# Kernel optimization log

Hardware: AMD Instinct MI355X
Metric: run time of the kernel (lower is better)

## Reference

```python
import jax, jax.numpy as jnp
import numpy as np

GROUPS = 32
EPS = 1e-5
N_HEADS = 4


def group_norm(x, w, b):
    # x: [B, C, T]; GroupNorm over (C/G, T) within each of G groups
    B, C, T = x.shape
    xg = x.reshape(B, GROUPS, (C // GROUPS) * T)
    mean = xg.mean(axis=-1, keepdims=True)
    var = xg.var(axis=-1, keepdims=True)
    xn = ((xg - mean) * jax.lax.rsqrt(var + EPS)).reshape(B, C, T)
    return xn * w[None, :, None] + b[None, :, None]


def setup_inputs() -> dict:
    key = jax.random.key(0)
    ks = jax.random.split(key, 5)
    B, C, H, W = 2, 256, 64, 64
    x = jax.random.normal(ks[0], (B, C, H, W), dtype=jnp.float32)
    norm_w = jnp.ones((C,), dtype=jnp.float32)
    norm_b = jnp.zeros((C,), dtype=jnp.float32)
    qkv_w = jax.random.normal(ks[1], (3 * C, C), dtype=jnp.float32) * (C ** -0.5)
    qkv_b = jax.random.normal(ks[2], (3 * C,), dtype=jnp.float32) * 0.02
    proj_w = jax.random.normal(ks[3], (C, C), dtype=jnp.float32) * (C ** -0.5)
    proj_b = jax.random.normal(ks[4], (C,), dtype=jnp.float32) * 0.02
    return {"x": x, "norm_w": norm_w, "norm_b": norm_b,
            "qkv_w": qkv_w, "qkv_b": qkv_b,
            "proj_w": proj_w, "proj_b": proj_b}


def reference(x, norm_w, norm_b, qkv_w, qkv_b, proj_w, proj_b):
    B, C, Hs, Ws = x.shape
    T = Hs * Ws
    xf = x.reshape(B, C, T)
    xn = group_norm(xf, norm_w, norm_b)
    # 1x1 conv1d == channel matmul: [3C,C] x [B,C,T] -> [B,3C,T]
    qkv = jnp.einsum('oc,bct->bot', qkv_w, xn) + qkv_b[None, :, None]
    ch = C // N_HEADS
    # legacy order: [B, H*3*ch, T] -> [B*H, 3*ch, T] -> split
    qkv_h = qkv.reshape(B * N_HEADS, 3 * ch, T)
    q, k, v = qkv_h[:, :ch], qkv_h[:, ch:2 * ch], qkv_h[:, 2 * ch:]
    scale = ch ** -0.25
    # full [B*H, T, T] score matrix, softmax in fp32 (faithful to source)
    weight = jnp.einsum('bct,bcs->bts', q * scale, k * scale)
    weight = jax.nn.softmax(weight.astype(jnp.float32), axis=-1).astype(qkv.dtype)
    a = jnp.einsum('bts,bcs->bct', weight, v).reshape(B, C, T)
    h = jnp.einsum('oc,bct->bot', proj_w, a) + proj_b[None, :, None]
    return (xf + h).reshape(B, C, Hs, Ws)
```

## Files before the change

kernel.cpp:

```cpp
#include <hip/hip_runtime.h>
#include <hip/hip_bf16.h>

#define B_    2
#define C_    256
#define T_    4096
#define GRP   32
#define CPG   8
#define NH    4
#define CH    64
#define K3C   768
#define SPLIT 4
#define GSL   8
#define NSTAT (B_ * GRP * GSL)
#define NCVT  128
#define LOG2E 1.4426950408889634f

typedef __attribute__((ext_vector_type(8))) short bf16x8;
typedef __attribute__((ext_vector_type(4))) float f32x4;

#if __has_builtin(__builtin_amdgcn_exp2f)
#define EXP2(x) __builtin_amdgcn_exp2f(x)
#else
#define EXP2(x) exp2f(x)
#endif

__device__ __forceinline__ unsigned pk2(float a, float b) {
    __hip_bfloat162 h = __float22bfloat162_rn(make_float2(a, b));
    union { __hip_bfloat162 h2; unsigned u; } cv; cv.h2 = h;
    return cv.u;
}
__device__ __forceinline__ float bf2f(unsigned short u) {
    return __uint_as_float((unsigned)u << 16);
}

__global__ __launch_bounds__(256) void pre_kernel(
    const float* __restrict__ x, float* __restrict__ stat,
    const float* __restrict__ qw, const float* __restrict__ pw,
    unsigned short* __restrict__ qwb, unsigned short* __restrict__ pwb) {
    int bid = blockIdx.x;
    int tid = threadIdx.x;
    if (bid < NSTAT) {
        int bg = bid >> 3, sl = bid & 7;
        const int SLN = CPG * T_ / GSL;
        const float* xp = x + (size_t)bg * CPG * T_ + (size_t)sl * SLN;
        float s = 0.f, s2 = 0.f;
        for (int i = tid * 4; i < SLN; i += 1024) {
            float4 v = *(const float4*)&xp[i];
            s  += (v.x + v.y) + (v.z + v.w);
            s2 += (v.x * v.x + v.y * v.y) + (v.z * v.z + v.w * v.w);
        }
        for (int off = 32; off > 0; off >>= 1) {
            s  += __shfl_down(s,  off);
            s2 += __shfl_down(s2, off);
        }
        __shared__ float rs[4], rs2[4];
        int wid = tid >> 6;
        if ((tid & 63) == 0) { rs[wid] = s; rs2[wid] = s2; }
        __syncthreads();
        if (tid == 0) {
            stat[bid * 2]     = (rs[0] + rs[1]) + (rs[2] + rs[3]);
            stat[bid * 2 + 1] = (rs2[0] + rs2[1]) + (rs2[2] + rs2[3]);
        }
    } else {
        int i = (bid - NSTAT) * 256 + tid;
        const int n1 = K3C * C_ / 8;
        const float* src; unsigned short* dst;
        if (i < n1) { src = qw + 8 * i; dst = qwb + 8 * i; }
        else { int j = i - n1; src = pw + 8 * j; dst = pwb + 8 * j; }
        float4 a = *(const float4*)src;
        float4 b = *(const float4*)(src + 4);
        uint4 u;
        u.x = pk2(a.x, a.y); u.y = pk2(a.z, a.w);
        u.z = pk2(b.x, b.y); u.w = pk2(b.z, b.w);
        *(uint4*)dst = u;
    }
}

__global__ __launch_bounds__(256) void gn_apply_kernel(
    const float* __restrict__ x, const float* __restrict__ stat,
    const float* __restrict__ w, const float* __restrict__ b,
    unsigned short* __restrict__ xnT) {
    int bg = blockIdx.x, sl = blockIdx.y;
    int batch = bg / GRP, g = bg % GRP;
    const float* xp = x + (size_t)bg * CPG * T_;
    int tid = threadIdx.x;

    float s = 0.f, s2 = 0.f;
#pragma unroll
    for (int i = 0; i < GSL; ++i) {
        s  += stat[(bg * GSL + i) * 2];
        s2 += stat[(bg * GSL + i) * 2 + 1];
    }
    float inv_n = 1.f / (float)(CPG * T_);
    float mean = s * inv_n;
    float var  = s2 * inv_n - mean * mean;
    float inv  = rsqrtf(var + 1e-5f);

    float wv[8], bv[8];
#pragma unroll
    for (int j = 0; j < 8; j++) {
        float ww = w[g * CPG + j] * inv;
        wv[j] = ww;
        bv[j] = b[g * CPG + j] - mean * ww;
    }
    unsigned short* op = xnT + (size_t)batch * T_ * C_ + g * CPG;
    int t0 = sl * (T_ / GSL);
#pragma unroll
    for (int rep = 0; rep < 2; ++rep) {
        int t = t0 + rep * 256 + tid;
        float v[8];
#pragma unroll
        for (int j = 0; j < 8; j++) v[j] = xp[(size_t)j * T_ + t] * wv[j] + bv[j];
        uint4 u;
        u.x = pk2(v[0], v[1]); u.y = pk2(v[2], v[3]);
        u.z = pk2(v[4], v[5]); u.w = pk2(v[6], v[7]);
        *(uint4*)&op[(size_t)t * C_] = u;
    }
}

__global__ __launch_bounds__(256) void qkv_gemm_kernel(
    const unsigned short* __restrict__ Wb, const float* __restrict__ bias,
    const unsigned short* __restrict__ Xt, unsigned short* __restrict__ q_t,
    unsigned short* __restrict__ k_t, unsigned short* __restrict__ v_d) {
    int tb = blockIdx.x * 128;
    int by = blockIdx.y;
    int bz = blockIdx.z;
    int ob = by * 64;
    int tid = threadIdx.x;
    int l = tid & 15, oct = (tid >> 4) & 3, w = tid >> 6;

    __shared__ __align__(16) unsigned short SH[64 * 264];

#pragma unroll
    for (int j = 0; j < 8; ++j) {
        int idx = tid + 256 * j;
        int row = idx >> 5, ch = idx & 31;
        *(uint4*)&SH[row * 264 + ch * 8] =
            *(const uint4*)&Wb[(size_t)(ob + row) * C_ + ch * 8];
    }
    __syncthreads();

    const unsigned short* Xb = Xt + (size_t)bz * T_ * C_;

    f32x4 acc[4][2];
#pragma unroll
    for (int mf = 0; mf < 4; ++mf)
#pragma unroll
        for (int nf = 0; nf < 2; ++nf) acc[mf][nf] = (f32x4){0.f, 0.f, 0.f, 0.f};

#pragma unroll
    for (int kk = 0; kk < 8; ++kk) {
        int c0 = 32 * kk + 8 * oct;
        bf16x8 bfr[2];
#pragma unroll
        for (int nf = 0; nf < 2; ++nf)
            bfr[nf] = *(const bf16x8*)&Xb[(size_t)(tb + 32 * w + 16 * nf + l) * C_ + c0];
#pragma unroll
        for (int mf = 0; mf < 4; ++mf) {
            bf16x8 af = *(const bf16x8*)&SH[(16 * mf + l) * 264 + c0];
#pragma unroll
            for (int nf = 0; nf < 2; ++nf)
                acc[mf][nf] = __builtin_amdgcn_mfma_f32_16x16x32_bf16(af, bfr[nf], acc[mf][nf], 0, 0, 0);
        }
    }

    int head = by / 3, sec = by - 3 * head;
    int bh = bz * NH + head;

    if (sec < 2) {
        float scale = (sec == 0) ? 0.125f * LOG2E : 1.f;
        unsigned short* dst = ((sec == 0) ? q_t : k_t) + (size_t)bh * T_ * CH;
#pragma unroll
        for (int mf = 0; mf < 4; ++mf) {
            float bvs[4];
#pragma unroll
            for (int r = 0; r < 4; ++r) bvs[r] = bias[ob + 16 * mf + 4 * oct + r];
#pragma unroll
            for (int nf = 0; nf < 2; ++nf) {
                int t = tb + 32 * w + 16 * nf + l;
                float v0 = (acc[mf][nf][0] + bvs[0]) * scale;
                float v1 = (acc[mf][nf][1] + bvs[1]) * scale;
                float v2 = (acc[mf][nf][2] + bvs[2]) * scale;
                float v3 = (acc[mf][nf][3] + bvs[3]) * scale;
                uint2 u; u.x = pk2(v0, v1); u.y = pk2(v2, v3);
                *(uint2*)&dst[(size_t)t * CH + 16 * mf + 4 * oct] = u;
            }
        }
    } else {
        __syncthreads();
#pragma unroll
        for (int mf = 0; mf < 4; ++mf) {
            float bvs[4];
#pragma unroll
            for (int r = 0; r < 4; ++r) bvs[r] = bias[ob + 16 * mf + 4 * oct + r];
#pragma unroll
            for (int nf = 0; nf < 2; ++nf) {
                int tl = 32 * w + 16 * nf + l;
#pragma unroll
                for (int r = 0; r < 4; ++r) {
                    unsigned pv = pk2(acc[mf][nf][r] + bvs[r], 0.f);
                    SH[(16 * mf + 4 * oct + r) * 136 + tl] = (unsigned short)(pv & 0xffffu);
                }
            }
        }
        __syncthreads();
        unsigned short* vdst = v_d + (size_t)bh * CH * T_;
#pragma unroll
        for (int j = 0; j < 4; ++j) {
            int idx = tid + 256 * j;
            int row = idx >> 4, ch = idx & 15;
            *(uint4*)&vdst[(size_t)row * T_ + tb + ch * 8] =
                *(uint4*)&SH[row * 136 + ch * 8];
        }
    }
}

__global__ __launch_bounds__(256, 4) void attn_kernel(
    const unsigned short* __restrict__ q_t, const unsigned short* __restrict__ k_t,
    const unsigned short* __restrict__ v_d, unsigned short* __restrict__ Opart,
    float* __restrict__ lbuf) {
    int bh = blockIdx.y;
    int sp = blockIdx.z;
    int t0 = blockIdx.x * 128;
    int tid = threadIdx.x;
    int l = tid & 15, q = (tid >> 4) & 3, w = tid >> 6;
    int lsw = l & 7;

    __shared__ __align__(16) unsigned short Kt[64 * 64];
    __shared__ __align__(16) unsigned short Vt[64 * 64];
    __shared__ __align__(16) unsigned short Ps[128 * 64];

    const unsigned short* qb = q_t + (size_t)bh * T_ * CH;
    const unsigned short* kb = k_t + (size_t)bh * T_ * CH;
    const unsigned short* vb = v_d + (size_t)bh * CH * T_;

    bf16x8 qf[2][2];
#pragma unroll
    for (int nf = 0; nf < 2; ++nf) {
        int t = t0 + 32 * w + 16 * nf + l;
#pragma unroll
        for (int kk = 0; kk < 2; ++kk)
            qf[nf][kk] = *(const bf16x8*)&qb[(size_t)t * CH + 32 * kk + 8 * q];
    }

    int srow = tid >> 3;
    int sch  = tid & 7;
    int ssw  = (sch ^ (srow & 7)) * 8;

    f32x4 O[4][2];
#pragma unroll
    for (int mf = 0; mf < 4; ++mf)
#pragma unroll
        for (int nf = 0; nf < 2; ++nf) O[mf][nf] = (f32x4){0.f, 0.f, 0.f, 0.f};
    float l_run[2] = {0.f, 0.f};

    int s_beg = sp * (T_ / SPLIT);
    int s_end = s_beg + (T_ / SPLIT);

    for (int s0 = s_beg; s0 < s_end; s0 += 64) {
        *(uint4*)&Kt[srow * 64 + ssw] =
            *(const uint4*)&kb[(size_t)(s0 + srow) * CH + sch * 8];
        *(uint4*)&Kt[(srow + 32) * 64 + ssw] =
            *(const uint4*)&kb[(size_t)(s0 + srow + 32) * CH + sch * 8];
        *(uint4*)&Vt[srow * 64 + ssw] =
            *(const uint4*)&vb[(size_t)srow * T_ + s0 + sch * 8];
        *(uint4*)&Vt[(srow + 32) * 64 + ssw] =
            *(const uint4*)&vb[(size_t)(srow + 32) * T_ + s0 + sch * 8];
        __syncthreads();

        f32x4 S[4][2];
#pragma unroll
        for (int sf = 0; sf < 4; ++sf) {
            f32x4 a0 = (f32x4){0.f, 0.f, 0.f, 0.f};
            f32x4 a1 = (f32x4){0.f, 0.f, 0.f, 0.f};
#pragma unroll
            for (int kk = 0; kk < 2; ++kk) {
                bf16x8 ka = *(const bf16x8*)
                    &Kt[(16 * sf + l) * 64 + (((4 * kk + q) ^ lsw) * 8)];
                a0 = __builtin_amdgcn_mfma_f32_16x16x32_bf16(ka, qf[0][kk], a0, 0, 0, 0);
                a1 = __builtin_amdgcn_mfma_f32_16x16x32_bf16(ka, qf[1][kk], a1, 0, 0, 0);
            }
            S[sf][0] = a0; S[sf][1] = a1;
        }

#pragma unroll
        for (int nf = 0; nf < 2; ++nf) {
            int trow = 32 * w + 16 * nf + l;
            float lloc = 0.f;
#pragma unroll
            for (int sf = 0; sf < 4; ++sf) {
                float p0 = EXP2(S[sf][nf][0]);
                float p1 = EXP2(S[sf][nf][1]);
                float p2 = EXP2(S[sf][nf][2]);
                float p3 = EXP2(S[sf][nf][3]);
                lloc += (p0 + p1) + (p2 + p3);
                uint2 u; u.x = pk2(p0, p1); u.y = pk2(p2, p3);
                *(uint2*)&Ps[trow * 64 + (((2 * sf + (q >> 1)) ^ lsw) * 8)
                             + (q & 1) * 4] = u;
            }
            l_run[nf] += lloc;
        }

#pragma unroll
        for (int kk = 0; kk < 2; ++kk) {
            bf16x8 pb[2];
#pragma unroll
            for (int nf = 0; nf < 2; ++nf)
                pb[nf] = *(const bf16x8*)
                    &Ps[(32 * w + 16 * nf + l) * 64 + (((4 * kk + q) ^ lsw) * 8)];
#pragma unroll
            for (int mf = 0; mf < 4; ++mf) {
                bf16x8 va = *(const bf16x8*)
                    &Vt[(16 * mf + l) * 64 + (((4 * kk + q) ^ lsw) * 8)];
#pragma unroll
                for (int nf = 0; nf < 2; ++nf)
                    O[mf][nf] = __builtin_amdgcn_mfma_f32_16x16x32_bf16(va, pb[nf], O[mf][nf], 0, 0, 0);
            }
        }
        __syncthreads();
    }

#pragma unroll
    for (int nf = 0; nf < 2; ++nf) {
        float lt = l_run[nf];
        lt += __shfl_xor(lt, 16);
        lt += __shfl_xor(lt, 32);
        float inv = 1.f / lt;
        int t = t0 + 32 * w + 16 * nf + l;
        size_t row = (size_t)(sp * 8 + bh) * T_ + t;
        unsigned short* op = Opart + row * CH;
#pragma unroll
        for (int mf = 0; mf < 4; ++mf) {
            uint2 u;
            u.x = pk2(O[mf][nf][0] * inv, O[mf][nf][1] * inv);
            u.y = pk2(O[mf][nf][2] * inv, O[mf][nf][3] * inv);
            *(uint2*)&op[16 * mf + 4 * q] = u;
        }
        if (q == 0) lbuf[row] = lt;
    }
}

__global__ __launch_bounds__(256) void combine_kernel(
    const unsigned short* __restrict__ Opart, const float* __restrict__ lbuf,
    unsigned short* __restrict__ a_t) {
    int bx = blockIdx.x;
    int bh = bx >> 6;
    int tblk = bx & 63;
    int tid = threadIdx.x;
    int t = tblk * 64 + (tid >> 2);
    int sub = tid & 3;

    float lw[SPLIT];
    size_t rows[SPLIT];
    float lsum = 0.f;
#pragma unroll
    for (int sp = 0; sp < SPLIT; ++sp) {
        rows[sp] = (size_t)(sp * 8 + bh) * T_ + t;
        lw[sp] = lbuf[rows[sp]];
        lsum += lw[sp];
    }
    float inv = 1.f / lsum;

    float o[16];
#pragma unroll
    for (int i = 0; i < 16; ++i) o[i] = 0.f;
#pragma unroll
    for (int sp = 0; sp < SPLIT; ++sp) {
        float s = lw[sp] * inv;
        const unsigned short* p = Opart + rows[sp] * CH + sub * 16;
        uint4 u0 = *(const uint4*)p;
        uint4 u1 = *(const uint4*)(p + 8);
        unsigned us[8] = {u0.x, u0.y, u0.z, u0.w, u1.x, u1.y, u1.z, u1.w};
#pragma unroll
        for (int j = 0; j < 8; ++j) {
            o[2 * j]     += bf2f((unsigned short)(us[j] & 0xffffu)) * s;
            o[2 * j + 1] += bf2f((unsigned short)(us[j] >> 16)) * s;
        }
    }

    int batch = bh >> 2, h = bh & 3;
    unsigned short* dst = a_t + ((size_t)batch * T_ + t) * C_ + h * CH + sub * 16;
    uint4 u0, u1;
    u0.x = pk2(o[0], o[1]);   u0.y = pk2(o[2], o[3]);
    u0.z = pk2(o[4], o[5]);   u0.w = pk2(o[6], o[7]);
    u1.x = pk2(o[8], o[9]);   u1.y = pk2(o[10], o[11]);
    u1.z = pk2(o[12], o[13]); u1.w = pk2(o[14], o[15]);
    *(uint4*)dst = u0;
    *(uint4*)(dst + 8) = u1;
}

__global__ __launch_bounds__(256) void proj_gemm_kernel(
    const unsigned short* __restrict__ Wb, const float* __restrict__ bias,
    const unsigned short* __restrict__ At, const float* __restrict__ xres,
    float* __restrict__ out) {
    int tb = blockIdx.x * 64;
    int ob = blockIdx.y * 64;
    int bz = blockIdx.z;
    int tid = threadIdx.x;
    int l = tid & 15, oct = (tid >> 4) & 3, w = tid >> 6;

    __shared__ __align__(16) unsigned short SH[64 * 264];

#pragma unroll
    for (int j = 0; j < 8; ++j) {
        int idx = tid + 256 * j;
        int row = idx >> 5, ch = idx & 31;
        *(uint4*)&SH[row * 264 + ch * 8] =
            *(const uint4*)&Wb[(size_t)(ob + row) * C_ + ch * 8];
    }
    __syncthreads();

    const unsigned short* Ab = At + (size_t)bz * T_ * C_;
    int t = tb + 16 * w + l;

    f32x4 acc[4];
#pragma unroll
    for (int mf = 0; mf < 4; ++mf) acc[mf] = (f32x4){0.f, 0.f, 0.f, 0.f};

#pragma unroll
    for (int kk = 0; kk < 8; ++kk) {
        int c0 = 32 * kk + 8 * oct;
        bf16x8 bfr = *(const bf16x8*)&Ab[(size_t)t * C_ + c0];
#pragma unroll
        for (int mf = 0; mf < 4; ++mf) {
            bf16x8 af = *(const bf16x8*)&SH[(16 * mf + l) * 264 + c0];
            acc[mf] = __builtin_amdgcn_mfma_f32_16x16x32_bf16(af, bfr, acc[mf], 0, 0, 0);
        }
    }

#pragma unroll
    for (int mf = 0; mf < 4; ++mf) {
#pragma unroll
        for (int r = 0; r < 4; ++r) {
            int o = ob + 16 * mf + 4 * oct + r;
            size_t idx = ((size_t)bz * C_ + o) * T_ + t;
            out[idx] = acc[mf][r] + bias[o] + xres[idx];
        }
    }
}

extern "C" void kernel_launch(void* const* d_in, const int* in_sizes, int n_in,
                              void* d_out, int out_size, void* d_ws, size_t ws_size,
                              hipStream_t stream) {
    const float* x      = (const float*)d_in[0];
    const float* norm_w = (const float*)d_in[1];
    const float* norm_b = (const float*)d_in[2];
    const float* qkv_w  = (const float*)d_in[3];
    const float* qkv_b  = (const float*)d_in[4];
    const float* proj_w = (const float*)d_in[5];
    const float* proj_b = (const float*)d_in[6];
    float* out = (float*)d_out;

    char* p = (char*)d_ws;
    unsigned short* xnT = (unsigned short*)p; p += (size_t)B_ * T_ * C_ * 2;
    unsigned short* qwb = (unsigned short*)p; p += (size_t)K3C * C_ * 2;
    unsigned short* pwb = (unsigned short*)p; p += (size_t)C_ * C_ * 2;
    unsigned short* q_t = (unsigned short*)p; p += (size_t)B_ * NH * T_ * CH * 2;
    unsigned short* k_t = (unsigned short*)p; p += (size_t)B_ * NH * T_ * CH * 2;
    unsigned short* v_d = (unsigned short*)p; p += (size_t)B_ * NH * T_ * CH * 2;
    unsigned short* Opart = (unsigned short*)p; p += (size_t)SPLIT * 8 * T_ * CH * 2;
    float* lbuf         = (float*)p;          p += (size_t)SPLIT * 8 * T_ * 4;
    unsigned short* a_t = (unsigned short*)p; p += (size_t)B_ * T_ * C_ * 2;
    float* stat         = (float*)p;          p += (size_t)NSTAT * 2 * 4;

    pre_kernel<<<dim3(NSTAT + NCVT), dim3(256), 0, stream>>>(
        x, stat, qkv_w, proj_w, qwb, pwb);
    gn_apply_kernel<<<dim3(B_ * GRP, GSL), dim3(256), 0, stream>>>(
        x, stat, norm_w, norm_b, xnT);
    qkv_gemm_kernel<<<dim3(T_ / 128, 12, B_), dim3(256), 0, stream>>>(
        qwb, qkv_b, xnT, q_t, k_t, v_d);
    attn_kernel<<<dim3(T_ / 128, B_ * NH, SPLIT), dim3(256), 0, stream>>>(
        q_t, k_t, v_d, Opart, lbuf);
    combine_kernel<<<dim3(B_ * NH * (T_ / 64)), dim3(256), 0, stream>>>(Opart, lbuf, a_t);
    proj_gemm_kernel<<<dim3(T_ / 64, C_ / 64, B_), dim3(256), 0, stream>>>(
        pwb, proj_b, a_t, x, out);
}
```

Baseline: 145.8 us.

## Load K/V fragments directly from global, remap attention grid per XCD, double split

The attention kernel no longer stages K and V tiles through shared memory. Each wave now loads its MFMA fragments straight from global memory, which removes both per-iteration __syncthreads barriers. The launch becomes a flattened 1D grid whose block index is decoded so that the blocks sharing one (head, split) pair land on the same XCD, aiming for better L2 reuse of K/V. SPLIT goes from 4 to 8 to double the block count. In exchange, every wave re-reads the same K/V data through the cache hierarchy instead of sharing one LDS copy, and the combine step has twice as many partials to merge.

```diff
diff --git a/kernel.cpp b/kernel.cpp
--- a/kernel.cpp
+++ b/kernel.cpp
@@ -9,7 +9,7 @@
 #define NH    4
 #define CH    64
 #define K3C   768
-#define SPLIT 4
+#define SPLIT 8
 #define GSL   8
 #define NSTAT (B_ * GRP * GSL)
 #define NCVT  128
@@ -219,15 +219,19 @@
     const unsigned short* __restrict__ q_t, const unsigned short* __restrict__ k_t,
     const unsigned short* __restrict__ v_d, unsigned short* __restrict__ Opart,
     float* __restrict__ lbuf) {
-    int bh = blockIdx.y;
-    int sp = blockIdx.z;
-    int t0 = blockIdx.x * 128;
+    int id = blockIdx.x;
+    int xcd = id & 7;
+    int j = id >> 3;
+    int pair = 8 * (j >> 5) + xcd;
+    int bx = j & 31;
+    int bh = pair >> 3;
+    int sp = pair & 7;
+    int t0 = bx * 128;
+
     int tid = threadIdx.x;
     int l = tid & 15, q = (tid >> 4) & 3, w = tid >> 6;
     int lsw = l & 7;
 
-    __shared__ __align__(16) unsigned short Kt[64 * 64];
-    __shared__ __align__(16) unsigned short Vt[64 * 64];
     __shared__ __align__(16) unsigned short Ps[128 * 64];
 
     const unsigned short* qb = q_t + (size_t)bh * T_ * CH;
@@ -243,10 +247,6 @@
             qf[nf][kk] = *(const bf16x8*)&qb[(size_t)t * CH + 32 * kk + 8 * q];
     }
 
-    int srow = tid >> 3;
-    int sch  = tid & 7;
-    int ssw  = (sch ^ (srow & 7)) * 8;
-
     f32x4 O[4][2];
 #pragma unroll
     for (int mf = 0; mf < 4; ++mf)
@@ -258,16 +258,6 @@
     int s_end = s_beg + (T_ / SPLIT);
 
     for (int s0 = s_beg; s0 < s_end; s0 += 64) {
-        *(uint4*)&Kt[srow * 64 + ssw] =
-            *(const uint4*)&kb[(size_t)(s0 + srow) * CH + sch * 8];
-        *(uint4*)&Kt[(srow + 32) * 64 + ssw] =
-            *(const uint4*)&kb[(size_t)(s0 + srow + 32) * CH + sch * 8];
-        *(uint4*)&Vt[srow * 64 + ssw] =
-            *(const uint4*)&vb[(size_t)srow * T_ + s0 + sch * 8];
-        *(uint4*)&Vt[(srow + 32) * 64 + ssw] =
-            *(const uint4*)&vb[(size_t)(srow + 32) * T_ + s0 + sch * 8];
-        __syncthreads();
-
         f32x4 S[4][2];
 #pragma unroll
         for (int sf = 0; sf < 4; ++sf) {
@@ -276,7 +266,7 @@
 #pragma unroll
             for (int kk = 0; kk < 2; ++kk) {
                 bf16x8 ka = *(const bf16x8*)
-                    &Kt[(16 * sf + l) * 64 + (((4 * kk + q) ^ lsw) * 8)];
+                    &kb[(size_t)(s0 + 16 * sf + l) * CH + 32 * kk + 8 * q];
                 a0 = __builtin_amdgcn_mfma_f32_16x16x32_bf16(ka, qf[0][kk], a0, 0, 0, 0);
                 a1 = __builtin_amdgcn_mfma_f32_16x16x32_bf16(ka, qf[1][kk], a1, 0, 0, 0);
             }
@@ -311,13 +301,12 @@
 #pragma unroll
             for (int mf = 0; mf < 4; ++mf) {
                 bf16x8 va = *(const bf16x8*)
-                    &Vt[(16 * mf + l) * 64 + (((4 * kk + q) ^ lsw) * 8)];
+                    &vb[(size_t)(16 * mf + l) * T_ + s0 + 32 * kk + 8 * q];
 #pragma unroll
                 for (int nf = 0; nf < 2; ++nf)
                     O[mf][nf] = __builtin_amdgcn_mfma_f32_16x16x32_bf16(va, pb[nf], O[mf][nf], 0, 0, 0);
             }
         }
-        __syncthreads();
     }
 
 #pragma unroll
@@ -469,7 +458,7 @@
         x, stat, norm_w, norm_b, xnT);
     qkv_gemm_kernel<<<dim3(T_ / 128, 12, B_), dim3(256), 0, stream>>>(
         qwb, qkv_b, xnT, q_t, k_t, v_d);
-    attn_kernel<<<dim3(T_ / 128, B_ * NH, SPLIT), dim3(256), 0, stream>>>(
+    attn_kernel<<<dim3((T_ / 128) * B_ * NH * SPLIT), dim3(256), 0, stream>>>(
         q_t, k_t, v_d, Opart, lbuf);
     combine_kernel<<<dim3(B_ * NH * (T_ / 64)), dim3(256), 0, stream>>>(Opart, lbuf, a_t);
     proj_gemm_kernel<<<dim3(T_ / 64, C_ / 64, B_), dim3(256), 0, stream>>>(
```

After: 228.1 us. 56.5% more time.

## Double-buffer K/V tiles in attention via direct global-to-LDS loads

Applied to the files above, without the earlier changes.

Loads K and V tiles into double-buffered shared memory with global_load_lds, prefetching the next tile while the current one is consumed. This replaces the register-staged load that stalled before every barrier. It also raises wave priority around the MFMA blocks and lowers the occupancy target from 4 to 3 blocks per CU to fit the larger LDS footprint. The direct-to-LDS path depends on the per-lane swizzled global addresses matching the LDS layout, and the lower occupancy reduces latency hiding.

```diff
diff --git a/kernel.cpp b/kernel.cpp
--- a/kernel.cpp
+++ b/kernel.cpp
@@ -33,6 +33,13 @@
     return __uint_as_float((unsigned)u << 16);
 }
 
+__device__ __forceinline__ void gl_lds16(const unsigned short* g, unsigned short* l) {
+    __builtin_amdgcn_global_load_lds(
+        (const __attribute__((address_space(1))) unsigned int*)g,
+        (__attribute__((address_space(3))) unsigned int*)l,
+        16, 0, 0);
+}
+
 __global__ __launch_bounds__(256) void pre_kernel(
     const float* __restrict__ x, float* __restrict__ stat,
     const float* __restrict__ qw, const float* __restrict__ pw,
@@ -215,7 +222,7 @@
     }
 }
 
-__global__ __launch_bounds__(256, 4) void attn_kernel(
+__global__ __launch_bounds__(256, 3) void attn_kernel(
     const unsigned short* __restrict__ q_t, const unsigned short* __restrict__ k_t,
     const unsigned short* __restrict__ v_d, unsigned short* __restrict__ Opart,
     float* __restrict__ lbuf) {
@@ -226,8 +233,8 @@
     int l = tid & 15, q = (tid >> 4) & 3, w = tid >> 6;
     int lsw = l & 7;
 
-    __shared__ __align__(16) unsigned short Kt[64 * 64];
-    __shared__ __align__(16) unsigned short Vt[64 * 64];
+    __shared__ __align__(16) unsigned short Kt[2][64 * 64];
+    __shared__ __align__(16) unsigned short Vt[2][64 * 64];
     __shared__ __align__(16) unsigned short Ps[128 * 64];
 
     const unsigned short* qb = q_t + (size_t)bh * T_ * CH;
@@ -243,9 +250,17 @@
             qf[nf][kk] = *(const bf16x8*)&qb[(size_t)t * CH + 32 * kk + 8 * q];
     }
 
-    int srow = tid >> 3;
-    int sch  = tid & 7;
-    int ssw  = (sch ^ (srow & 7)) * 8;
+    int ln = tid & 63;
+    int rsub = ln >> 3;
+    int cm8 = ((ln & 7) ^ rsub) * 8;
+    int kr0 = 16 * w + rsub;
+
+#define STAGE(buf, s0) do {                                                    \
+    gl_lds16(kb + (size_t)((s0) + kr0) * CH + cm8,     &Kt[buf][(16 * w) * 64]);     \
+    gl_lds16(kb + (size_t)((s0) + kr0 + 8) * CH + cm8, &Kt[buf][(16 * w + 8) * 64]); \
+    gl_lds16(vb + (size_t)kr0 * T_ + (s0) + cm8,       &Vt[buf][(16 * w) * 64]);     \
+    gl_lds16(vb + (size_t)(kr0 + 8) * T_ + (s0) + cm8, &Vt[buf][(16 * w + 8) * 64]); \
+} while (0)
 
     f32x4 O[4][2];
 #pragma unroll
@@ -255,20 +270,18 @@
     float l_run[2] = {0.f, 0.f};
 
     int s_beg = sp * (T_ / SPLIT);
-    int s_end = s_beg + (T_ / SPLIT);
-
-    for (int s0 = s_beg; s0 < s_end; s0 += 64) {
-        *(uint4*)&Kt[srow * 64 + ssw] =
-            *(const uint4*)&kb[(size_t)(s0 + srow) * CH + sch * 8];
-        *(uint4*)&Kt[(srow + 32) * 64 + ssw] =
-            *(const uint4*)&kb[(size_t)(s0 + srow + 32) * CH + sch * 8];
-        *(uint4*)&Vt[srow * 64 + ssw] =
-            *(const uint4*)&vb[(size_t)srow * T_ + s0 + sch * 8];
-        *(uint4*)&Vt[(srow + 32) * 64 + ssw] =
-            *(const uint4*)&vb[(size_t)(srow + 32) * T_ + s0 + sch * 8];
-        __syncthreads();
+    const int NT = (T_ / SPLIT) / 64;
+
+    STAGE(0, s_beg);
+    __syncthreads();
+
+    int cur = 0;
+    for (int t = 0; t < NT; ++t) {
+        int s0n = s_beg + (t + 1) * 64;
+        if (t + 1 < NT) STAGE(cur ^ 1, s0n);
 
         f32x4 S[4][2];
+        __builtin_amdgcn_s_setprio(1);
 #pragma unroll
         for (int sf = 0; sf < 4; ++sf) {
             f32x4 a0 = (f32x4){0.f, 0.f, 0.f, 0.f};
@@ -276,12 +289,13 @@
 #pragma unroll
             for (int kk = 0; kk < 2; ++kk) {
                 bf16x8 ka = *(const bf16x8*)
-                    &Kt[(16 * sf + l) * 64 + (((4 * kk + q) ^ lsw) * 8)];
+                    &Kt[cur][(16 * sf + l) * 64 + (((4 * kk + q) ^ lsw) * 8)];
                 a0 = __builtin_amdgcn_mfma_f32_16x16x32_bf16(ka, qf[0][kk], a0, 0, 0, 0);
                 a1 = __builtin_amdgcn_mfma_f32_16x16x32_bf16(ka, qf[1][kk], a1, 0, 0, 0);
             }
             S[sf][0] = a0; S[sf][1] = a1;
         }
+        __builtin_amdgcn_s_setprio(0);
 
 #pragma unroll
         for (int nf = 0; nf < 2; ++nf) {
@@ -308,17 +322,21 @@
             for (int nf = 0; nf < 2; ++nf)
                 pb[nf] = *(const bf16x8*)
                     &Ps[(32 * w + 16 * nf + l) * 64 + (((4 * kk + q) ^ lsw) * 8)];
+            __builtin_amdgcn_s_setprio(1);
 #pragma unroll
             for (int mf = 0; mf < 4; ++mf) {
                 bf16x8 va = *(const bf16x8*)
-                    &Vt[(16 * mf + l) * 64 + (((4 * kk + q) ^ lsw) * 8)];
+                    &Vt[cur][(16 * mf + l) * 64 + (((4 * kk + q) ^ lsw) * 8)];
 #pragma unroll
                 for (int nf = 0; nf < 2; ++nf)
                     O[mf][nf] = __builtin_amdgcn_mfma_f32_16x16x32_bf16(va, pb[nf], O[mf][nf], 0, 0, 0);
             }
+            __builtin_amdgcn_s_setprio(0);
         }
         __syncthreads();
-    }
+        cur ^= 1;
+    }
+#undef STAGE
 
 #pragma unroll
     for (int nf = 0; nf < 2; ++nf) {
```

Measured after the change: 149.7 us. +2.7%, slower.
